# Optimization experiments

Hardware: AMD Instinct MI355X
Metric: run time of the kernel (lower is better)

The kernel has to match this reference:

```python
import jax, jax.numpy as jnp
import numpy as np

N_NODES = 200000  # num_users + num_items
N_EDGES = 500000
LATENT = 64
N_LAYERS = 3
NEG_SLOPE = 0.01  # F.leaky_relu default
EPS = 1e-16       # PyG geo_softmax denominator epsilon


def setup_inputs() -> dict:
    key = jax.random.key(0)
    k1, k2, k3, k4, k5 = jax.random.split(key, 5)
    edge_index = jax.random.randint(k1, (2, N_EDGES), 0, N_NODES, dtype=jnp.int64 if jax.config.jax_enable_x64 else jnp.int32)
    edge_attrs = jax.random.normal(k2, (N_EDGES, 2), dtype=jnp.float32)
    emb = jax.random.normal(k3, (N_NODES, LATENT), dtype=jnp.float32)
    # per-layer attention params, shape [L, heads=1 -> squeezed, in_channels]
    a_att_w = jax.random.normal(k4, (N_LAYERS, LATENT), dtype=jnp.float32) * 0.1
    r_att_w = jax.random.normal(k5, (N_LAYERS, LATENT), dtype=jnp.float32) * 0.1
    return {"edge_index": edge_index, "edge_attrs": edge_attrs, "emb": emb,
            "a_att_w": a_att_w, "r_att_w": r_att_w}


def _segment_softmax(scores, dst, num_nodes):
    # scores: [E, D] softmax over edges grouped by destination node (PyG geo_softmax)
    m = jax.ops.segment_max(scores, dst, num_segments=num_nodes)  # [N, D]
    m = jnp.where(jnp.isfinite(m), m, 0.0)  # nodes without incoming edges
    w = jnp.exp(scores - m[dst])
    den = jax.ops.segment_sum(w, dst, num_segments=num_nodes)     # [N, D]
    return w / (den[dst] + EPS)


def reference(edge_index, edge_attrs, emb, a_att_w, r_att_w):
    src, dst = edge_index[0], edge_index[1]
    n = emb.shape[0]
    # symmetric degree normalization (degree of destination endpoints)
    deg = jax.ops.segment_sum(jnp.ones_like(dst, dtype=emb.dtype), dst, num_segments=n)
    dinv = jnp.where(deg > 0, deg ** -0.5, 0.0)
    norm = (dinv[src] * dinv[dst])[:, None]  # [E, 1]

    a_e = edge_attrs[:, 0:1]  # [E, 1]
    r_e = edge_attrs[:, 1:2]

    x = emb
    acc = emb  # layer-0 embedding
    for l in range(N_LAYERS):
        scores = (jax.nn.leaky_relu(a_e * a_att_w[l], NEG_SLOPE)
                  + jax.nn.leaky_relu(r_e * r_att_w[l], NEG_SLOPE))  # [E, D]
        attn = _segment_softmax(scores, dst, n)                       # [E, D]
        msg = norm * attn * x[src]                                    # gather + weight
        x = jax.ops.segment_sum(msg, dst, num_segments=n)             # scatter-add
        acc = acc + x
    out = acc / (N_LAYERS + 1)  # mean over layer embeddings
    return out
```

## Files before the change

kernel.cpp:

```cpp
#include <hip/hip_runtime.h>

#define BLK 256
#define LBLK 256

__device__ __forceinline__ unsigned short f2bf(float f) {
    unsigned u = __float_as_uint(f);
    u += 0x7FFFu + ((u >> 16) & 1u);
    return (unsigned short)(u >> 16);
}
__device__ __forceinline__ float bf2f(unsigned short h) {
    return __uint_as_float((unsigned)h << 16);
}
__device__ __forceinline__ float4 unpack4(ushort4 h) {
    return make_float4(bf2f(h.x), bf2f(h.y), bf2f(h.z), bf2f(h.w));
}
__device__ __forceinline__ ushort4 pack4(float4 f) {
    ushort4 h; h.x = f2bf(f.x); h.y = f2bf(f.y); h.z = f2bf(f.z); h.w = f2bf(f.w);
    return h;
}


__global__ void k_deg(const int* __restrict__ dst, int* __restrict__ deg,
                      int* __restrict__ rank, int E) {
    int e = blockIdx.x * blockDim.x + threadIdx.x;
    if (e < E) rank[e] = atomicAdd(&deg[dst[e]], 1);
}

__global__ void k_scan1(const int* __restrict__ deg, int* __restrict__ partials,
                        int N, int chunk) {
    __shared__ int sm[BLK];
    int b = blockIdx.x;
    int start = b * chunk;
    int end = min(start + chunk, N);
    int s = 0;
    for (int i = start + threadIdx.x; i < end; i += BLK) s += deg[i];
    sm[threadIdx.x] = s;
    __syncthreads();
    for (int off = BLK / 2; off > 0; off >>= 1) {
        if (threadIdx.x < off) sm[threadIdx.x] += sm[threadIdx.x + off];
        __syncthreads();
    }
    if (threadIdx.x == 0) partials[b] = sm[0];
}

__global__ void k_scan23(const int* __restrict__ deg, const int* __restrict__ partials,
                         int* __restrict__ row_off, int N, int E, int chunk) {
    __shared__ int sp[BLK];
    __shared__ int sm[BLK];
    int b = blockIdx.x;
    int t = threadIdx.x;
    sp[t] = partials[t];
    __syncthreads();
    for (int off = 1; off < BLK; off <<= 1) {
        int add = (t >= off) ? sp[t - off] : 0;
        __syncthreads();
        sp[t] += add;
        __syncthreads();
    }
    int base = (b == 0) ? 0 : sp[b - 1];
    if (b == 0 && t == 0) row_off[N] = E;
    __syncthreads();
    int start = b * chunk;
    int end = min(start + chunk, N);
    for (int tile = start; tile < end; tile += BLK) {
        int idx = tile + t;
        int val = (idx < end) ? deg[idx] : 0;
        sm[t] = val;
        __syncthreads();
        for (int off = 1; off < BLK; off <<= 1) {
            int add = (t >= off) ? sm[t - off] : 0;
            __syncthreads();
            sm[t] += add;
            __syncthreads();
        }
        if (idx < end) row_off[idx] = base + sm[t] - val;
        int tile_total = sm[BLK - 1];
        __syncthreads();
        base += tile_total;
    }
}

__global__ void k_conv(const float4* __restrict__ emb4, const int* __restrict__ deg,
                       ushort4* __restrict__ embs, int N16) {
    int i = blockIdx.x * blockDim.x + threadIdx.x;
    if (i >= N16) return;
    int v = i >> 4;
    int d = deg[v];
    float dinv = (d > 0) ? rsqrtf((float)d) : 0.0f;
    float4 e = emb4[i];
    embs[i] = pack4(make_float4(dinv * e.x, dinv * e.y, dinv * e.z, dinv * e.w));
}

__global__ void k_fill(const int* __restrict__ src, const int* __restrict__ dst,
                       const float* __restrict__ attrs, const int* __restrict__ row_off,
                       const int* __restrict__ rank, float4* __restrict__ csr, int E) {
    int e = blockIdx.x * blockDim.x + threadIdx.x;
    if (e >= E) return;
    int pos = row_off[dst[e]] + rank[e];
    float2 ar = ((const float2*)attrs)[e];
    csr[pos] = make_float4(__int_as_float(src[e]), ar.x, ar.y, 0.0f);
}


__device__ __forceinline__ float lrelu(float x) { return x > 0.0f ? x : 0.01f * x; }

__device__ __forceinline__ float4 edge_w4(float a, float r, const float4& aw, const float4& rw) {
    float4 w;
    w.x = __expf(lrelu(a * aw.x) + lrelu(r * rw.x));
    w.y = __expf(lrelu(a * aw.y) + lrelu(r * rw.y));
    w.z = __expf(lrelu(a * aw.z) + lrelu(r * rw.z));
    w.w = __expf(lrelu(a * aw.w) + lrelu(r * rw.w));
    return w;
}

template<int MODE>
__global__ __launch_bounds__(LBLK) void k_layer(
    const ushort4* __restrict__ xs, const float4* __restrict__ csr,
    const int* __restrict__ row_off, const int* __restrict__ deg,
    const float4* __restrict__ aw4, const float4* __restrict__ rw4,
    const float4* __restrict__ emb4,
    const ushort4* __restrict__ xsA, const ushort4* __restrict__ xsB,
    ushort4* __restrict__ xsout, float4* __restrict__ out4, int N) {
    const int t = threadIdx.x;
    const int d4 = t & 15;
    const int v = blockIdx.x * (LBLK / 16) + (t >> 4);
    if (v >= N) return;
    const float4 aw = aw4[d4];
    const float4 rw = rw4[d4];
    const int s0 = row_off[v];
    const int s1 = row_off[v + 1];
    const int dv = deg[v];
    float4 num = {0.f, 0.f, 0.f, 0.f};
    float4 den = {0.f, 0.f, 0.f, 0.f};
    for (int i = s0; i < s1; i += 2) {
        const int last = s1 - 1;
        float4 e0 = csr[i];
        float4 e1 = csr[min(i + 1, last)];
        ushort4 h0 = xs[(size_t)(unsigned)__float_as_int(e0.x) * 16 + d4];
        ushort4 h1 = xs[(size_t)(unsigned)__float_as_int(e1.x) * 16 + d4];
        float4 w0 = edge_w4(e0.y, e0.z, aw, rw);
        float4 w1 = edge_w4(e1.y, e1.z, aw, rw);
        float g1 = (i + 1 < s1) ? 1.0f : 0.0f;
        w1.x *= g1; w1.y *= g1; w1.z *= g1; w1.w *= g1;
        float4 x0 = unpack4(h0);
        float4 x1 = unpack4(h1);
        den.x += w0.x + w1.x; den.y += w0.y + w1.y;
        den.z += w0.z + w1.z; den.w += w0.w + w1.w;
        num.x += w0.x * x0.x + w1.x * x1.x;
        num.y += w0.y * x0.y + w1.y * x1.y;
        num.z += w0.z * x0.z + w1.z * x1.z;
        num.w += w0.w * x0.w + w1.w * x1.w;
    }
    float4 xr;
    xr.x = num.x / (den.x + 1e-16f);
    xr.y = num.y / (den.y + 1e-16f);
    xr.z = num.z / (den.z + 1e-16f);
    xr.w = num.w / (den.w + 1e-16f);
    const float dinv = (dv > 0) ? rsqrtf((float)dv) : 0.0f;
    const size_t o = (size_t)v * 16 + d4;
    if (MODE == 2) {
        const float sd = (dv > 0) ? sqrtf((float)dv) : 0.0f;
        float4 e = emb4[o];
        float4 A = unpack4(xsA[o]);
        float4 B = unpack4(xsB[o]);
        float4 r;
        r.x = (e.x + sd * (A.x + B.x) + dinv * xr.x) * 0.25f;
        r.y = (e.y + sd * (A.y + B.y) + dinv * xr.y) * 0.25f;
        r.z = (e.z + sd * (A.z + B.z) + dinv * xr.z) * 0.25f;
        r.w = (e.w + sd * (A.w + B.w) + dinv * xr.w) * 0.25f;
        out4[o] = r;
    } else {
        const float s = dinv * dinv;
        xsout[o] = pack4(make_float4(s * xr.x, s * xr.y, s * xr.z, s * xr.w));
    }
}


extern "C" void kernel_launch(void* const* d_in, const int* in_sizes, int n_in,
                              void* d_out, int out_size, void* d_ws, size_t ws_size,
                              hipStream_t stream) {
    const int*   ei    = (const int*)d_in[0];
    const float* attrs = (const float*)d_in[1];
    const float* emb   = (const float*)d_in[2];
    const float* a_att = (const float*)d_in[3];
    const float* r_att = (const float*)d_in[4];

    const int E = in_sizes[0] / 2;
    const int N = in_sizes[2] / 64;
    const int* src = ei;
    const int* dst = ei + E;

    char* ws = (char*)d_ws;
    size_t off = 0;
    auto alloc = [&](size_t bytes) {
        void* p = ws + off;
        off += (bytes + 255) & ~(size_t)255;
        return p;
    };
    int*     deg      = (int*)alloc((size_t)N * 4);
    int*     rank     = (int*)alloc((size_t)E * 4);
    int*     row_off  = (int*)alloc((size_t)(N + 1) * 4);
    int*     partials = (int*)alloc((size_t)BLK * 4);
    float4*  csr      = (float4*)alloc((size_t)E * 16);
    ushort4* embs     = (ushort4*)alloc((size_t)N * 16 * 8);
    ushort4* xsA      = (ushort4*)alloc((size_t)N * 16 * 8);
    ushort4* xsB      = (ushort4*)alloc((size_t)N * 16 * 8);
    float4*  out      = (float4*)d_out;

    hipMemsetAsync(deg, 0, (size_t)N * 4, stream);

    int gE = (E + BLK - 1) / BLK;
    int chunk = (N + BLK - 1) / BLK;

    k_deg   <<<gE, BLK, 0, stream>>>(dst, deg, rank, E);
    k_scan1 <<<BLK, BLK, 0, stream>>>(deg, partials, N, chunk);
    k_scan23<<<BLK, BLK, 0, stream>>>(deg, partials, row_off, N, E, chunk);
    k_conv  <<<(N * 16 + BLK - 1) / BLK, BLK, 0, stream>>>((const float4*)emb, deg, embs, N * 16);
    k_fill  <<<gE, BLK, 0, stream>>>(src, dst, attrs, row_off, rank, csr, E);

    const float4* emb4 = (const float4*)emb;
    const float4* aw4  = (const float4*)a_att;
    const float4* rw4  = (const float4*)r_att;

    int gL = (N + (LBLK / 16) - 1) / (LBLK / 16);
    k_layer<0><<<gL, LBLK, 0, stream>>>(embs, csr, row_off, deg, aw4,      rw4,
                                        nullptr, nullptr, nullptr, xsA, nullptr, N);
    k_layer<1><<<gL, LBLK, 0, stream>>>(xsA,  csr, row_off, deg, aw4 + 16, rw4 + 16,
                                        nullptr, nullptr, nullptr, xsB, nullptr, N);
    k_layer<2><<<gL, LBLK, 0, stream>>>(xsB,  csr, row_off, deg, aw4 + 32, rw4 + 32,
                                        emb4, xsA, xsB, nullptr, out, N);
}
```

Measured before the change: 257.1 us.

## Widen scan, fuse conv+fill, pack CSR to 8 bytes, unroll edge loop by four

The two-pass prefix scan now uses 1024-element chunks with int4 loads, replacing the serial per-block tile loop. The conversion and CSR-fill kernels are merged into one launch. CSR entries shrink from 16 to 8 bytes by storing the edge attributes as packed bf16, which cuts gather bandwidth but reduces the precision of the attention inputs. The layer kernel now takes degree from row offsets, unrolls the edge loop by four for more memory-level parallelism, and uses fmaxf for leaky-relu.

```diff
diff --git a/kernel.cpp b/kernel.cpp
--- a/kernel.cpp
+++ b/kernel.cpp
@@ -2,6 +2,7 @@
 
 #define BLK 256
 #define LBLK 256
+#define CH 1024
 
 __device__ __forceinline__ unsigned short f2bf(float f) {
     unsigned u = __float_as_uint(f);
@@ -26,30 +27,31 @@
     if (e < E) rank[e] = atomicAdd(&deg[dst[e]], 1);
 }
 
-__global__ void k_scan1(const int* __restrict__ deg, int* __restrict__ partials,
-                        int N, int chunk) {
+__global__ void k_scan1(const int* __restrict__ deg, int* __restrict__ partials, int N) {
     __shared__ int sm[BLK];
-    int b = blockIdx.x;
-    int start = b * chunk;
-    int end = min(start + chunk, N);
+    int i0 = blockIdx.x * CH + threadIdx.x * 4;
     int s = 0;
-    for (int i = start + threadIdx.x; i < end; i += BLK) s += deg[i];
+    if (i0 + 3 < N) {
+        int4 v = *(const int4*)(deg + i0);
+        s = (v.x + v.y) + (v.z + v.w);
+    } else {
+        for (int k = 0; k < 4; ++k) if (i0 + k < N) s += deg[i0 + k];
+    }
     sm[threadIdx.x] = s;
     __syncthreads();
     for (int off = BLK / 2; off > 0; off >>= 1) {
         if (threadIdx.x < off) sm[threadIdx.x] += sm[threadIdx.x + off];
         __syncthreads();
     }
-    if (threadIdx.x == 0) partials[b] = sm[0];
-}
-
-__global__ void k_scan23(const int* __restrict__ deg, const int* __restrict__ partials,
-                         int* __restrict__ row_off, int N, int E, int chunk) {
+    if (threadIdx.x == 0) partials[blockIdx.x] = sm[0];
+}
+
+__global__ void k_scan2(const int* __restrict__ deg, const int* __restrict__ partials,
+                        int* __restrict__ row_off, int N, int E, int nb) {
     __shared__ int sp[BLK];
     __shared__ int sm[BLK];
-    int b = blockIdx.x;
-    int t = threadIdx.x;
-    sp[t] = partials[t];
+    int b = blockIdx.x, t = threadIdx.x;
+    sp[t] = (t < nb) ? partials[t] : 0;
     __syncthreads();
     for (int off = 1; off < BLK; off <<= 1) {
         int add = (t >= off) ? sp[t - off] : 0;
@@ -59,52 +61,69 @@
     }
     int base = (b == 0) ? 0 : sp[b - 1];
     if (b == 0 && t == 0) row_off[N] = E;
+    int i0 = b * CH + t * 4;
+    int v0 = 0, v1 = 0, v2 = 0, v3 = 0;
+    if (i0 + 3 < N) {
+        int4 v = *(const int4*)(deg + i0);
+        v0 = v.x; v1 = v.y; v2 = v.z; v3 = v.w;
+    } else {
+        if (i0     < N) v0 = deg[i0];
+        if (i0 + 1 < N) v1 = deg[i0 + 1];
+        if (i0 + 2 < N) v2 = deg[i0 + 2];
+    }
+    int tot = (v0 + v1) + (v2 + v3);
+    sm[t] = tot;
     __syncthreads();
-    int start = b * chunk;
-    int end = min(start + chunk, N);
-    for (int tile = start; tile < end; tile += BLK) {
-        int idx = tile + t;
-        int val = (idx < end) ? deg[idx] : 0;
-        sm[t] = val;
-        __syncthreads();
-        for (int off = 1; off < BLK; off <<= 1) {
-            int add = (t >= off) ? sm[t - off] : 0;
-            __syncthreads();
-            sm[t] += add;
-            __syncthreads();
-        }
-        if (idx < end) row_off[idx] = base + sm[t] - val;
-        int tile_total = sm[BLK - 1];
-        __syncthreads();
-        base += tile_total;
-    }
-}
-
-__global__ void k_conv(const float4* __restrict__ emb4, const int* __restrict__ deg,
-                       ushort4* __restrict__ embs, int N16) {
-    int i = blockIdx.x * blockDim.x + threadIdx.x;
-    if (i >= N16) return;
-    int v = i >> 4;
-    int d = deg[v];
-    float dinv = (d > 0) ? rsqrtf((float)d) : 0.0f;
-    float4 e = emb4[i];
-    embs[i] = pack4(make_float4(dinv * e.x, dinv * e.y, dinv * e.z, dinv * e.w));
-}
-
-__global__ void k_fill(const int* __restrict__ src, const int* __restrict__ dst,
-                       const float* __restrict__ attrs, const int* __restrict__ row_off,
-                       const int* __restrict__ rank, float4* __restrict__ csr, int E) {
-    int e = blockIdx.x * blockDim.x + threadIdx.x;
-    if (e >= E) return;
-    int pos = row_off[dst[e]] + rank[e];
-    float2 ar = ((const float2*)attrs)[e];
-    csr[pos] = make_float4(__int_as_float(src[e]), ar.x, ar.y, 0.0f);
-}
-
-
-__device__ __forceinline__ float lrelu(float x) { return x > 0.0f ? x : 0.01f * x; }
-
-__device__ __forceinline__ float4 edge_w4(float a, float r, const float4& aw, const float4& rw) {
+    for (int off = 1; off < BLK; off <<= 1) {
+        int add = (t >= off) ? sm[t - off] : 0;
+        __syncthreads();
+        sm[t] += add;
+        __syncthreads();
+    }
+    int excl = base + sm[t] - tot;
+    int4 r;
+    r.x = excl;
+    r.y = excl + v0;
+    r.z = excl + v0 + v1;
+    r.w = excl + v0 + v1 + v2;
+    if (i0 + 3 < N) {
+        *(int4*)(row_off + i0) = r;
+    } else {
+        if (i0     < N) row_off[i0]     = r.x;
+        if (i0 + 1 < N) row_off[i0 + 1] = r.y;
+        if (i0 + 2 < N) row_off[i0 + 2] = r.z;
+    }
+}
+
+__global__ void k_convfill(const int* __restrict__ src, const int* __restrict__ dst,
+                           const float2* __restrict__ attrs, const int* __restrict__ row_off,
+                           const int* __restrict__ rank, const int* __restrict__ deg,
+                           uint2* __restrict__ csr, const float4* __restrict__ emb4,
+                           ushort4* __restrict__ embs, int E, int N16, int gF) {
+    int b = blockIdx.x;
+    if (b < gF) {
+        int e = b * BLK + threadIdx.x;
+        if (e >= E) return;
+        int pos = row_off[dst[e]] + rank[e];
+        float2 ar = attrs[e];
+        csr[pos] = make_uint2((unsigned)src[e],
+                              (unsigned)f2bf(ar.x) | ((unsigned)f2bf(ar.y) << 16));
+    } else {
+        int i = (b - gF) * BLK + threadIdx.x;
+        if (i >= N16) return;
+        int d = deg[i >> 4];
+        float dinv = (d > 0) ? rsqrtf((float)d) : 0.0f;
+        float4 e = emb4[i];
+        embs[i] = pack4(make_float4(dinv * e.x, dinv * e.y, dinv * e.z, dinv * e.w));
+    }
+}
+
+
+__device__ __forceinline__ float lrelu(float x) { return fmaxf(x, 0.01f * x); }
+
+__device__ __forceinline__ float4 edge_w4(unsigned ar, const float4& aw, const float4& rw) {
+    float a = bf2f((unsigned short)(ar & 0xffffu));
+    float r = bf2f((unsigned short)(ar >> 16));
     float4 w;
     w.x = __expf(lrelu(a * aw.x) + lrelu(r * rw.x));
     w.y = __expf(lrelu(a * aw.y) + lrelu(r * rw.y));
@@ -113,10 +132,20 @@
     return w;
 }
 
+__device__ __forceinline__ void acc4(float4& num, float4& den,
+                                     const float4& w, const ushort4& h, float g) {
+    float4 x = unpack4(h);
+    den.x += g * w.x; den.y += g * w.y; den.z += g * w.z; den.w += g * w.w;
+    num.x += g * w.x * x.x;
+    num.y += g * w.y * x.y;
+    num.z += g * w.z * x.z;
+    num.w += g * w.w * x.w;
+}
+
 template<int MODE>
 __global__ __launch_bounds__(LBLK) void k_layer(
-    const ushort4* __restrict__ xs, const float4* __restrict__ csr,
-    const int* __restrict__ row_off, const int* __restrict__ deg,
+    const ushort4* __restrict__ xs, const uint2* __restrict__ csr,
+    const int* __restrict__ row_off,
     const float4* __restrict__ aw4, const float4* __restrict__ rw4,
     const float4* __restrict__ emb4,
     const ushort4* __restrict__ xsA, const ushort4* __restrict__ xsB,
@@ -129,27 +158,30 @@
     const float4 rw = rw4[d4];
     const int s0 = row_off[v];
     const int s1 = row_off[v + 1];
-    const int dv = deg[v];
+    const int dv = s1 - s0;
     float4 num = {0.f, 0.f, 0.f, 0.f};
     float4 den = {0.f, 0.f, 0.f, 0.f};
-    for (int i = s0; i < s1; i += 2) {
+    for (int i = s0; i < s1; i += 4) {
         const int last = s1 - 1;
-        float4 e0 = csr[i];
-        float4 e1 = csr[min(i + 1, last)];
-        ushort4 h0 = xs[(size_t)(unsigned)__float_as_int(e0.x) * 16 + d4];
-        ushort4 h1 = xs[(size_t)(unsigned)__float_as_int(e1.x) * 16 + d4];
-        float4 w0 = edge_w4(e0.y, e0.z, aw, rw);
-        float4 w1 = edge_w4(e1.y, e1.z, aw, rw);
+        uint2 e0 = csr[i];
+        uint2 e1 = csr[min(i + 1, last)];
+        uint2 e2 = csr[min(i + 2, last)];
+        uint2 e3 = csr[min(i + 3, last)];
+        ushort4 h0 = xs[(size_t)e0.x * 16 + d4];
+        ushort4 h1 = xs[(size_t)e1.x * 16 + d4];
+        ushort4 h2 = xs[(size_t)e2.x * 16 + d4];
+        ushort4 h3 = xs[(size_t)e3.x * 16 + d4];
+        float4 w0 = edge_w4(e0.y, aw, rw);
+        float4 w1 = edge_w4(e1.y, aw, rw);
+        float4 w2 = edge_w4(e2.y, aw, rw);
+        float4 w3 = edge_w4(e3.y, aw, rw);
         float g1 = (i + 1 < s1) ? 1.0f : 0.0f;
-        w1.x *= g1; w1.y *= g1; w1.z *= g1; w1.w *= g1;
-        float4 x0 = unpack4(h0);
-        float4 x1 = unpack4(h1);
-        den.x += w0.x + w1.x; den.y += w0.y + w1.y;
-        den.z += w0.z + w1.z; den.w += w0.w + w1.w;
-        num.x += w0.x * x0.x + w1.x * x1.x;
-        num.y += w0.y * x0.y + w1.y * x1.y;
-        num.z += w0.z * x0.z + w1.z * x1.z;
-        num.w += w0.w * x0.w + w1.w * x1.w;
+        float g2 = (i + 2 < s1) ? 1.0f : 0.0f;
+        float g3 = (i + 3 < s1) ? 1.0f : 0.0f;
+        acc4(num, den, w0, h0, 1.0f);
+        acc4(num, den, w1, h1, g1);
+        acc4(num, den, w2, h2, g2);
+        acc4(num, den, w3, h3, g3);
     }
     float4 xr;
     xr.x = num.x / (den.x + 1e-16f);
@@ -201,7 +233,7 @@
     int*     rank     = (int*)alloc((size_t)E * 4);
     int*     row_off  = (int*)alloc((size_t)(N + 1) * 4);
     int*     partials = (int*)alloc((size_t)BLK * 4);
-    float4*  csr      = (float4*)alloc((size_t)E * 16);
+    uint2*   csr      = (uint2*)alloc((size_t)E * 8);
     ushort4* embs     = (ushort4*)alloc((size_t)N * 16 * 8);
     ushort4* xsA      = (ushort4*)alloc((size_t)N * 16 * 8);
     ushort4* xsB      = (ushort4*)alloc((size_t)N * 16 * 8);
@@ -210,23 +242,26 @@
     hipMemsetAsync(deg, 0, (size_t)N * 4, stream);
 
     int gE = (E + BLK - 1) / BLK;
-    int chunk = (N + BLK - 1) / BLK;
-
-    k_deg   <<<gE, BLK, 0, stream>>>(dst, deg, rank, E);
-    k_scan1 <<<BLK, BLK, 0, stream>>>(deg, partials, N, chunk);
-    k_scan23<<<BLK, BLK, 0, stream>>>(deg, partials, row_off, N, E, chunk);
-    k_conv  <<<(N * 16 + BLK - 1) / BLK, BLK, 0, stream>>>((const float4*)emb, deg, embs, N * 16);
-    k_fill  <<<gE, BLK, 0, stream>>>(src, dst, attrs, row_off, rank, csr, E);
+    int nb = (N + CH - 1) / CH;
+    int gF = gE;
+    int gC = (N * 16 + BLK - 1) / BLK;
+
+    k_deg     <<<gE, BLK, 0, stream>>>(dst, deg, rank, E);
+    k_scan1   <<<nb, BLK, 0, stream>>>(deg, partials, N);
+    k_scan2   <<<nb, BLK, 0, stream>>>(deg, partials, row_off, N, E, nb);
+    k_convfill<<<gF + gC, BLK, 0, stream>>>(src, dst, (const float2*)attrs, row_off,
+                                            rank, deg, csr, (const float4*)emb,
+                                            embs, E, N * 16, gF);
 
     const float4* emb4 = (const float4*)emb;
     const float4* aw4  = (const float4*)a_att;
     const float4* rw4  = (const float4*)r_att;
 
     int gL = (N + (LBLK / 16) - 1) / (LBLK / 16);
-    k_layer<0><<<gL, LBLK, 0, stream>>>(embs, csr, row_off, deg, aw4,      rw4,
+    k_layer<0><<<gL, LBLK, 0, stream>>>(embs, csr, row_off, aw4,      rw4,
                                         nullptr, nullptr, nullptr, xsA, nullptr, N);
-    k_layer<1><<<gL, LBLK, 0, stream>>>(xsA,  csr, row_off, deg, aw4 + 16, rw4 + 16,
+    k_layer<1><<<gL, LBLK, 0, stream>>>(xsA,  csr, row_off, aw4 + 16, rw4 + 16,
                                         nullptr, nullptr, nullptr, xsB, nullptr, N);
-    k_layer<2><<<gL, LBLK, 0, stream>>>(xsB,  csr, row_off, deg, aw4 + 32, rw4 + 32,
+    k_layer<2><<<gL, LBLK, 0, stream>>>(xsB,  csr, row_off, aw4 + 32, rw4 + 32,
                                         emb4, xsA, xsB, nullptr, out, N);
 }
```

Measured after the change: 242.2 us. -5.8%, faster.
